# Optimization experiments

Measured on AMD Instinct MI355X. Metric: run time of the kernel, lower is better.

## Reference

```python
import jax, jax.numpy as jnp
import numpy as np

B, S, D = 16, 2048, 128

def setup_inputs() -> dict:
    key = jax.random.key(0)
    kq, kk, kv, km = jax.random.split(key, 4)
    Q = jax.random.normal(kq, (B, S, D), dtype=jnp.float32)
    K = jax.random.normal(kk, (B, S, D), dtype=jnp.float32)
    V = jax.random.normal(kv, (B, S, D), dtype=jnp.float32)
    # mask: True entries are masked out (filled with -inf), same as torch.masked_fill_
    mask = jax.random.randint(km, (B, S, S), 0, 2).astype(bool)
    return {"Q": Q, "K": K, "V": V, "mask": mask, "dk": 128}

def reference(Q, K, V, mask, dk):
    # scores: [B, S_q, S_k]
    w = jnp.einsum('bqd,bkd->bqk', Q, K)
    w = jnp.where(mask, -jnp.inf, w)
    # scale applied to masked scores (as in original: mask first, then divide);
    # -inf / scale stays -inf, so math matches exactly.
    scale = jnp.asarray(dk, w.dtype) ** 0.5
    p = jax.nn.softmax(w / scale, axis=-1)
    # context: [B, S_q, D]
    return jnp.einsum('bqk,bkd->bqd', p, V)
```

## Files before the change

### kernel.cpp

```cpp
#include <hip/hip_runtime.h>
#include <hip/hip_bf16.h>
#include <stdint.h>

typedef __attribute__((ext_vector_type(8))) short short8;
typedef __attribute__((ext_vector_type(4))) float floatx4;

#define S_LEN 2048
#define DH    128
#define BQ    64
#define BKV   64
#define NSTEP (S_LEN / BKV)
#define SCALE 0.08838834764831845f

__device__ __forceinline__ unsigned short f2b(float f) {
    union { float f; unsigned u; } v; v.f = f;
    unsigned r = v.u + 0x7fffu + ((v.u >> 16) & 1u);
    return (unsigned short)(r >> 16);
}

#define LDS_BYTES 77824

__global__ __launch_bounds__(256, 2)
void attn_fwd(const float* __restrict__ Q, const float* __restrict__ K,
              const float* __restrict__ V, const int* __restrict__ M,
              float* __restrict__ O)
{
    __shared__ __align__(128) char lds[LDS_BYTES];

    const int tid  = threadIdx.x;
    const int lane = tid & 63;
    const int w    = tid >> 6;
    const int c    = lane & 15;
    const int g    = lane >> 4;
    const int qt   = blockIdx.x;
    const int b    = blockIdx.y;
    const int q0   = qt * BQ;

    const int rbase = tid >> 5;
    const int c4    = tid & 31;
    const unsigned swk = (unsigned)(c4 * 8) ^ (unsigned)(rbase << 4);
    const int vd    = tid & 127;
    const int vk0   = (tid >> 7) * 32;

    short8 qf[4];
    {
        const float* qrow = Q + ((size_t)(b * S_LEN + q0 + w * 16 + c)) * DH;
        #pragma unroll
        for (int dk = 0; dk < 4; ++dk) {
            const float* p = qrow + dk * 32 + g * 8;
            float4 a  = *(const float4*)(p);
            float4 bb = *(const float4*)(p + 4);
            short8 f;
            f[0] = f2b(a.x * SCALE);  f[1] = f2b(a.y * SCALE);
            f[2] = f2b(a.z * SCALE);  f[3] = f2b(a.w * SCALE);
            f[4] = f2b(bb.x * SCALE); f[5] = f2b(bb.y * SCALE);
            f[6] = f2b(bb.z * SCALE); f[7] = f2b(bb.w * SCALE);
            qf[dk] = f;
        }
    }

    float m_run[4] = {-1e30f, -1e30f, -1e30f, -1e30f};
    float l_run[4] = {0.f, 0.f, 0.f, 0.f};
    floatx4 accO[8];
    #pragma unroll
    for (int i = 0; i < 8; ++i) accO[i] = (floatx4)(0.f);

    const float* Kb = K + (size_t)b * S_LEN * DH;
    const float* Vb = V + (size_t)b * S_LEN * DH;
    const int*   Mb = M + (size_t)b * S_LEN * S_LEN + (size_t)q0 * S_LEN;

    size_t moff[4];
    #pragma unroll
    for (int r = 0; r < 4; ++r)
        moff[r] = (size_t)(w * 16 + 4 * g + r) * S_LEN;

    float4 kreg[8];
    float  vreg[32];
    int    mreg[16];

    #pragma unroll
    for (int i = 0; i < 8; ++i)
        kreg[i] = *(const float4*)(Kb + (size_t)(i * 8 + rbase) * DH + c4 * 4);
    #pragma unroll
    for (int j = 0; j < 32; ++j)
        vreg[j] = Vb[(size_t)(vk0 + j) * DH + vd];
    #pragma unroll
    for (int r = 0; r < 4; ++r)
        #pragma unroll
        for (int n = 0; n < 4; ++n)
            mreg[r * 4 + n] = Mb[moff[r] + n * 16 + c];

    #pragma unroll
    for (int i = 0; i < 8; ++i) {
        float4 kv = kreg[i];
        unsigned long long kp =
              (unsigned long long)f2b(kv.x)
            | ((unsigned long long)f2b(kv.y) << 16)
            | ((unsigned long long)f2b(kv.z) << 32)
            | ((unsigned long long)f2b(kv.w) << 48);
        *(unsigned long long*)(lds + (i * 8 + rbase) * 256 + swk) = kp;
    }
    {
        char* vbase = lds + 32768 + vd * 144 + vk0 * 2;
        #pragma unroll
        for (int i = 0; i < 4; ++i) {
            short8 pk;
            #pragma unroll
            for (int e = 0; e < 8; ++e) pk[e] = f2b(vreg[i * 8 + e]);
            *(short8*)(vbase + i * 16) = pk;
        }
    }
    #pragma unroll
    for (int i = 0; i < 8; ++i)
        kreg[i] = *(const float4*)(Kb + (size_t)(BKV + i * 8 + rbase) * DH + c4 * 4);
    #pragma unroll
    for (int j = 0; j < 32; ++j)
        vreg[j] = Vb[(size_t)(BKV + vk0 + j) * DH + vd];

    __syncthreads();

    char* psw = lds + 69632 + w * 2048;

    for (int step = 0; step < NSTEP; ++step) {
        const int p = step & 1;
        const int kv0 = step * BKV;
        char* KHp = lds + p * 16384;
        char* VTp = lds + 32768 + p * 18432;

        floatx4 accS[4];
        #pragma unroll
        for (int n = 0; n < 4; ++n) accS[n] = (floatx4)(0.f);
        #pragma unroll
        for (int n = 0; n < 4; ++n) {
            const char* krow = KHp + (n * 16 + c) * 256;
            #pragma unroll
            for (int dk = 0; dk < 4; ++dk) {
                unsigned colb = (unsigned)(dk * 64 + g * 16) ^ (unsigned)((c & 7) << 4);
                short8 kf = *(const short8*)(krow + colb);
                accS[n] = __builtin_amdgcn_mfma_f32_16x16x32_bf16(qf[dk], kf, accS[n], 0, 0, 0);
            }
        }

        float pv[4][4];
        float corr[4];
        #pragma unroll
        for (int r = 0; r < 4; ++r) {
            float sv[4];
            #pragma unroll
            for (int n = 0; n < 4; ++n) {
                float s = accS[n][r];
                if (mreg[r * 4 + n]) s = -1e30f;
                sv[n] = s;
            }
            float tm = fmaxf(fmaxf(sv[0], sv[1]), fmaxf(sv[2], sv[3]));
            #pragma unroll
            for (int off = 1; off < 16; off <<= 1)
                tm = fmaxf(tm, __shfl_xor(tm, off, 64));
            float mn = fmaxf(m_run[r], tm);
            corr[r]  = __expf(m_run[r] - mn);
            m_run[r] = mn;
            float ts = 0.f;
            #pragma unroll
            for (int n = 0; n < 4; ++n) { pv[n][r] = __expf(sv[n] - mn); ts += pv[n][r]; }
            #pragma unroll
            for (int off = 1; off < 16; off <<= 1)
                ts += __shfl_xor(ts, off, 64);
            l_run[r] = l_run[r] * corr[r] + ts;
        }
        if (step + 1 < NSTEP) {
            const int kvn = kv0 + BKV;
            #pragma unroll
            for (int r = 0; r < 4; ++r)
                #pragma unroll
                for (int n = 0; n < 4; ++n)
                    mreg[r * 4 + n] = Mb[moff[r] + kvn + n * 16 + c];
        }

        #pragma unroll
        for (int s8 = 0; s8 < 8; ++s8) {
            floatx4 o = accO[s8];
            o[0] *= corr[0]; o[1] *= corr[1]; o[2] *= corr[2]; o[3] *= corr[3];
            accO[s8] = o;
        }

        #pragma unroll
        for (int r = 0; r < 4; ++r) {
            int rl = 4 * g + r;
            #pragma unroll
            for (int n = 0; n < 4; ++n) {
                unsigned colb = (unsigned)((n * 16 + c) * 2) ^ (unsigned)((rl & 7) << 4);
                *(unsigned short*)(psw + rl * 128 + colb) = f2b(pv[n][r]);
            }
        }

        #pragma unroll
        for (int sub = 0; sub < 2; ++sub) {
            unsigned colb = (unsigned)(sub * 64 + g * 16) ^ (unsigned)((c & 7) << 4);
            short8 pf = *(const short8*)(psw + c * 128 + colb);
            #pragma unroll
            for (int s8 = 0; s8 < 8; ++s8) {
                short8 vf = *(const short8*)(VTp + (s8 * 16 + c) * 144 + sub * 64 + g * 16);
                accO[s8] = __builtin_amdgcn_mfma_f32_16x16x32_bf16(pf, vf, accO[s8], 0, 0, 0);
            }
        }

        if (step + 1 < NSTEP) {
            char* KHn = lds + (p ^ 1) * 16384;
            char* VTn = lds + 32768 + (p ^ 1) * 18432;
            #pragma unroll
            for (int i = 0; i < 8; ++i) {
                float4 kv = kreg[i];
                unsigned long long kp =
                      (unsigned long long)f2b(kv.x)
                    | ((unsigned long long)f2b(kv.y) << 16)
                    | ((unsigned long long)f2b(kv.z) << 32)
                    | ((unsigned long long)f2b(kv.w) << 48);
                *(unsigned long long*)(KHn + (i * 8 + rbase) * 256 + swk) = kp;
            }
            char* vbase = VTn + vd * 144 + vk0 * 2;
            #pragma unroll
            for (int i = 0; i < 4; ++i) {
                short8 pk;
                #pragma unroll
                for (int e = 0; e < 8; ++e) pk[e] = f2b(vreg[i * 8 + e]);
                *(short8*)(vbase + i * 16) = pk;
            }
            if (step + 2 < NSTEP) {
                const int kvn2 = kv0 + 2 * BKV;
                #pragma unroll
                for (int i = 0; i < 8; ++i)
                    kreg[i] = *(const float4*)(Kb + (size_t)(kvn2 + i * 8 + rbase) * DH + c4 * 4);
                #pragma unroll
                for (int j = 0; j < 32; ++j)
                    vreg[j] = Vb[(size_t)(kvn2 + vk0 + j) * DH + vd];
            }
        }
        __syncthreads();
    }

    float inv[4];
    #pragma unroll
    for (int r = 0; r < 4; ++r) inv[r] = (l_run[r] > 0.f) ? 1.f / l_run[r] : 0.f;
    float* Ob = O + ((size_t)(b * S_LEN + q0 + w * 16)) * DH;
    #pragma unroll
    for (int s8 = 0; s8 < 8; ++s8) {
        #pragma unroll
        for (int r = 0; r < 4; ++r) {
            Ob[(size_t)(4 * g + r) * DH + s8 * 16 + c] = accO[s8][r] * inv[r];
        }
    }
}

extern "C" void kernel_launch(void* const* d_in, const int* in_sizes, int n_in,
                              void* d_out, int out_size, void* d_ws, size_t ws_size,
                              hipStream_t stream) {
    const float* Q = (const float*)d_in[0];
    const float* K = (const float*)d_in[1];
    const float* V = (const float*)d_in[2];
    const int*   M = (const int*)d_in[3];
    float*       O = (float*)d_out;
    dim3 grid(S_LEN / BQ, 16);
    attn_fwd<<<grid, dim3(256), 0, stream>>>(Q, K, V, M, O);
}
```

Baseline: 131.7 us.

## Pre-convert K to bf16 and pre-transpose V, stream K via global_load_lds

Adds two prep kernels: one converts K to bf16 and one transposes V into a bf16 d-major layout, both written to workspace. The attention kernel then loads K straight into swizzled LDS with global_load_lds double buffering and copies V^T tiles without per-element conversion. This halves K/V bytes re-read by every query tile and removes conversion work from the inner loop, at the cost of two extra launches and a pass over K/V. The old kernel is kept as a fallback when the workspace is too small.

```diff
diff --git a/kernel.cpp b/kernel.cpp
--- a/kernel.cpp
+++ b/kernel.cpp
@@ -18,11 +18,45 @@
     return (unsigned short)(r >> 16);
 }
 
+__device__ __forceinline__ void gll16(const void* g, void* l) {
+    __builtin_amdgcn_global_load_lds(
+        (__attribute__((address_space(1))) void*)(g),
+        (__attribute__((address_space(3))) void*)(l), 16, 0, 0);
+}
+
+
+__global__ __launch_bounds__(256) void conv_k(const float* __restrict__ K,
+                                              unsigned short* __restrict__ Kbf)
+{
+    int i = blockIdx.x * 256 + threadIdx.x;
+    float4 v = ((const float4*)K)[i];
+    ushort4 o;
+    o.x = f2b(v.x); o.y = f2b(v.y); o.z = f2b(v.z); o.w = f2b(v.w);
+    ((ushort4*)Kbf)[i] = o;
+}
+
+__global__ __launch_bounds__(256) void transp_v(const float* __restrict__ V,
+                                                unsigned short* __restrict__ Vt)
+{
+    __shared__ float t[32][33];
+    const int k0 = blockIdx.x * 32, d0 = blockIdx.y * 32, b = blockIdx.z;
+    const int tx = threadIdx.x & 31, ty = threadIdx.x >> 5;
+    const float* Vb = V + ((size_t)b * S_LEN + k0) * DH + d0;
+    #pragma unroll
+    for (int i = 0; i < 4; ++i)
+        t[ty + 8 * i][tx] = Vb[(size_t)(ty + 8 * i) * DH + tx];
+    __syncthreads();
+    unsigned short* Vtb = Vt + ((size_t)b * DH + d0) * S_LEN + k0;
+    #pragma unroll
+    for (int i = 0; i < 4; ++i)
+        Vtb[(size_t)(ty + 8 * i) * S_LEN + tx] = f2b(t[tx][ty + 8 * i]);
+}
+
 #define LDS_BYTES 77824
 
 __global__ __launch_bounds__(256, 2)
-void attn_fwd(const float* __restrict__ Q, const float* __restrict__ K,
-              const float* __restrict__ V, const int* __restrict__ M,
+void attn_fwd(const float* __restrict__ Q, const unsigned short* __restrict__ Kbf,
+              const unsigned short* __restrict__ Vt, const int* __restrict__ M,
               float* __restrict__ O)
 {
     __shared__ __align__(128) char lds[LDS_BYTES];
@@ -36,11 +70,8 @@
     const int b    = blockIdx.y;
     const int q0   = qt * BQ;
 
-    const int rbase = tid >> 5;
-    const int c4    = tid & 31;
-    const unsigned swk = (unsigned)(c4 * 8) ^ (unsigned)(rbase << 4);
-    const int vd    = tid & 127;
-    const int vk0   = (tid >> 7) * 32;
+    const int vd = tid & 127;
+    const int vh = tid >> 7;
 
     short8 qf[4];
     {
@@ -65,6 +96,216 @@
     #pragma unroll
     for (int i = 0; i < 8; ++i) accO[i] = (floatx4)(0.f);
 
+    const unsigned short* Kb  = Kbf + (size_t)b * S_LEN * DH;
+    const unsigned short* Vtb = Vt  + (size_t)b * DH * S_LEN;
+    const int*            Mb  = M   + (size_t)b * S_LEN * S_LEN + (size_t)q0 * S_LEN;
+
+    size_t moff[4];
+    #pragma unroll
+    for (int r = 0; r < 4; ++r)
+        moff[r] = (size_t)(w * 16 + 4 * g + r) * S_LEN;
+
+    short8 vreg[4];
+    int    mreg[16];
+
+    const int krow_l = lane >> 4;
+    const int kcol_l = (lane & 15) * 16;
+
+    #pragma unroll
+    for (int i = 0; i < 4; ++i) {
+        int j = (w << 2) | i;
+        int r = j * 4 + krow_l;
+        unsigned cb = (unsigned)kcol_l ^ (unsigned)((r & 7) << 4);
+        gll16((const char*)Kb + (size_t)r * 256 + cb, lds + j * 1024);
+    }
+    #pragma unroll
+    for (int j = 0; j < 4; ++j)
+        vreg[j] = *(const short8*)(Vtb + (size_t)vd * S_LEN + vh * 32 + j * 8);
+    #pragma unroll
+    for (int j = 0; j < 4; ++j)
+        *(short8*)(lds + 32768 + vd * 144 + vh * 64 + j * 16) = vreg[j];
+    #pragma unroll
+    for (int r = 0; r < 4; ++r)
+        #pragma unroll
+        for (int n = 0; n < 4; ++n)
+            mreg[r * 4 + n] = Mb[moff[r] + n * 16 + c];
+    #pragma unroll
+    for (int j = 0; j < 4; ++j)
+        vreg[j] = *(const short8*)(Vtb + (size_t)vd * S_LEN + BKV + vh * 32 + j * 8);
+
+    __syncthreads();
+
+    char* psw = lds + 69632 + w * 2048;
+
+    for (int step = 0; step < NSTEP; ++step) {
+        const int p = step & 1;
+        const int kv0 = step * BKV;
+        char* KHp = lds + p * 16384;
+        char* VTp = lds + 32768 + p * 18432;
+
+        if (step + 1 < NSTEP) {
+            const char* Ksrc = (const char*)Kb + (size_t)(kv0 + BKV) * 256;
+            char* KHn = lds + (p ^ 1) * 16384;
+            #pragma unroll
+            for (int i = 0; i < 4; ++i) {
+                int j = (w << 2) | i;
+                int r = j * 4 + krow_l;
+                unsigned cb = (unsigned)kcol_l ^ (unsigned)((r & 7) << 4);
+                gll16(Ksrc + (size_t)r * 256 + cb, KHn + j * 1024);
+            }
+        }
+
+        floatx4 accS[4];
+        #pragma unroll
+        for (int n = 0; n < 4; ++n) accS[n] = (floatx4)(0.f);
+        #pragma unroll
+        for (int n = 0; n < 4; ++n) {
+            const char* krow = KHp + (n * 16 + c) * 256;
+            #pragma unroll
+            for (int dk = 0; dk < 4; ++dk) {
+                unsigned colb = (unsigned)(dk * 64 + g * 16) ^ (unsigned)((c & 7) << 4);
+                short8 kf = *(const short8*)(krow + colb);
+                accS[n] = __builtin_amdgcn_mfma_f32_16x16x32_bf16(qf[dk], kf, accS[n], 0, 0, 0);
+            }
+        }
+
+        float pv[4][4];
+        float corr[4];
+        #pragma unroll
+        for (int r = 0; r < 4; ++r) {
+            float sv[4];
+            #pragma unroll
+            for (int n = 0; n < 4; ++n) {
+                float s = accS[n][r];
+                if (mreg[r * 4 + n]) s = -1e30f;
+                sv[n] = s;
+            }
+            float tm = fmaxf(fmaxf(sv[0], sv[1]), fmaxf(sv[2], sv[3]));
+            #pragma unroll
+            for (int off = 1; off < 16; off <<= 1)
+                tm = fmaxf(tm, __shfl_xor(tm, off, 64));
+            float mn = fmaxf(m_run[r], tm);
+            corr[r]  = __expf(m_run[r] - mn);
+            m_run[r] = mn;
+            float ts = 0.f;
+            #pragma unroll
+            for (int n = 0; n < 4; ++n) { pv[n][r] = __expf(sv[n] - mn); ts += pv[n][r]; }
+            #pragma unroll
+            for (int off = 1; off < 16; off <<= 1)
+                ts += __shfl_xor(ts, off, 64);
+            l_run[r] = l_run[r] * corr[r] + ts;
+        }
+        if (step + 1 < NSTEP) {
+            const int kvn = kv0 + BKV;
+            #pragma unroll
+            for (int r = 0; r < 4; ++r)
+                #pragma unroll
+                for (int n = 0; n < 4; ++n)
+                    mreg[r * 4 + n] = Mb[moff[r] + kvn + n * 16 + c];
+        }
+
+        #pragma unroll
+        for (int s8 = 0; s8 < 8; ++s8) {
+            floatx4 o = accO[s8];
+            o[0] *= corr[0]; o[1] *= corr[1]; o[2] *= corr[2]; o[3] *= corr[3];
+            accO[s8] = o;
+        }
+
+        #pragma unroll
+        for (int r = 0; r < 4; ++r) {
+            int rl = 4 * g + r;
+            #pragma unroll
+            for (int n = 0; n < 4; ++n) {
+                unsigned colb = (unsigned)((n * 16 + c) * 2) ^ (unsigned)((rl & 7) << 4);
+                *(unsigned short*)(psw + rl * 128 + colb) = f2b(pv[n][r]);
+            }
+        }
+
+        #pragma unroll
+        for (int sub = 0; sub < 2; ++sub) {
+            unsigned colb = (unsigned)(sub * 64 + g * 16) ^ (unsigned)((c & 7) << 4);
+            short8 pf = *(const short8*)(psw + c * 128 + colb);
+            #pragma unroll
+            for (int s8 = 0; s8 < 8; ++s8) {
+                short8 vf = *(const short8*)(VTp + (s8 * 16 + c) * 144 + sub * 64 + g * 16);
+                accO[s8] = __builtin_amdgcn_mfma_f32_16x16x32_bf16(pf, vf, accO[s8], 0, 0, 0);
+            }
+        }
+
+        if (step + 1 < NSTEP) {
+            char* VTn = lds + 32768 + (p ^ 1) * 18432;
+            #pragma unroll
+            for (int j = 0; j < 4; ++j)
+                *(short8*)(VTn + vd * 144 + vh * 64 + j * 16) = vreg[j];
+            if (step + 2 < NSTEP) {
+                const unsigned short* vsrc = Vtb + (size_t)vd * S_LEN + kv0 + 2 * BKV + vh * 32;
+                #pragma unroll
+                for (int j = 0; j < 4; ++j)
+                    vreg[j] = *(const short8*)(vsrc + j * 8);
+            }
+        }
+        __syncthreads();
+    }
+
+    float inv[4];
+    #pragma unroll
+    for (int r = 0; r < 4; ++r) inv[r] = (l_run[r] > 0.f) ? 1.f / l_run[r] : 0.f;
+    float* Ob = O + ((size_t)(b * S_LEN + q0 + w * 16)) * DH;
+    #pragma unroll
+    for (int s8 = 0; s8 < 8; ++s8) {
+        #pragma unroll
+        for (int r = 0; r < 4; ++r) {
+            Ob[(size_t)(4 * g + r) * DH + s8 * 16 + c] = accO[s8][r] * inv[r];
+        }
+    }
+}
+
+
+__global__ __launch_bounds__(256, 2)
+void attn_fwd_fb(const float* __restrict__ Q, const float* __restrict__ K,
+                 const float* __restrict__ V, const int* __restrict__ M,
+                 float* __restrict__ O)
+{
+    __shared__ __align__(128) char lds[LDS_BYTES];
+
+    const int tid  = threadIdx.x;
+    const int lane = tid & 63;
+    const int w    = tid >> 6;
+    const int c    = lane & 15;
+    const int g    = lane >> 4;
+    const int qt   = blockIdx.x;
+    const int b    = blockIdx.y;
+    const int q0   = qt * BQ;
+
+    const int rbase = tid >> 5;
+    const int c4    = tid & 31;
+    const unsigned swk = (unsigned)(c4 * 8) ^ (unsigned)(rbase << 4);
+    const int vd    = tid & 127;
+    const int vk0   = (tid >> 7) * 32;
+
+    short8 qf[4];
+    {
+        const float* qrow = Q + ((size_t)(b * S_LEN + q0 + w * 16 + c)) * DH;
+        #pragma unroll
+        for (int dk = 0; dk < 4; ++dk) {
+            const float* p = qrow + dk * 32 + g * 8;
+            float4 a  = *(const float4*)(p);
+            float4 bb = *(const float4*)(p + 4);
+            short8 f;
+            f[0] = f2b(a.x * SCALE);  f[1] = f2b(a.y * SCALE);
+            f[2] = f2b(a.z * SCALE);  f[3] = f2b(a.w * SCALE);
+            f[4] = f2b(bb.x * SCALE); f[5] = f2b(bb.y * SCALE);
+            f[6] = f2b(bb.z * SCALE); f[7] = f2b(bb.w * SCALE);
+            qf[dk] = f;
+        }
+    }
+
+    float m_run[4] = {-1e30f, -1e30f, -1e30f, -1e30f};
+    float l_run[4] = {0.f, 0.f, 0.f, 0.f};
+    floatx4 accO[8];
+    #pragma unroll
+    for (int i = 0; i < 8; ++i) accO[i] = (floatx4)(0.f);
+
     const float* Kb = K + (size_t)b * S_LEN * DH;
     const float* Vb = V + (size_t)b * S_LEN * DH;
     const int*   Mb = M + (size_t)b * S_LEN * S_LEN + (size_t)q0 * S_LEN;
@@ -259,6 +500,15 @@
     const float* V = (const float*)d_in[2];
     const int*   M = (const int*)d_in[3];
     float*       O = (float*)d_out;
-    dim3 grid(S_LEN / BQ, 16);
-    attn_fwd<<<grid, dim3(256), 0, stream>>>(Q, K, V, M, O);
-}
+
+    const size_t elems = (size_t)16 * S_LEN * DH;
+    if (ws_size >= 2 * elems * sizeof(unsigned short)) {
+        unsigned short* Kbf = (unsigned short*)d_ws;
+        unsigned short* Vt  = (unsigned short*)d_ws + elems;
+        conv_k<<<dim3((unsigned)(elems / 4 / 256)), dim3(256), 0, stream>>>(K, Kbf);
+        transp_v<<<dim3(S_LEN / 32, DH / 32, 16), dim3(256), 0, stream>>>(V, Vt);
+        attn_fwd<<<dim3(S_LEN / BQ, 16), dim3(256), 0, stream>>>(Q, Kbf, Vt, M, O);
+    } else {
+        attn_fwd_fb<<<dim3(S_LEN / BQ, 16), dim3(256), 0, stream>>>(Q, K, V, M, O);
+    }
+}
```

Measured after the change: 140.3 us. 6.5% more time.

## Pre-convert K to bf16 and transpose V into workspace, async-load K to LDS

Applied to the files above, without the earlier changes.

Adds two pre-pass kernels that convert K to bf16 and write V transposed in bf16 into the workspace. The main attention kernel then streams half-size operands, loads K tiles straight into swizzled LDS with global_load_lds double buffering, and keeps V and the mask in registers one or two steps ahead. It also uses a transposed QK^T MFMA layout so each lane owns one query row, which makes softmax reductions and output stores simpler. LDS use drops and occupancy rises to 3 blocks, at the cost of two extra launches and extra workspace traffic; the old kernel remains as a fallback when the workspace is too small.

```diff
diff --git a/kernel.cpp b/kernel.cpp
--- a/kernel.cpp
+++ b/kernel.cpp
@@ -18,11 +18,51 @@
     return (unsigned short)(r >> 16);
 }
 
-#define LDS_BYTES 77824
-
-__global__ __launch_bounds__(256, 2)
-void attn_fwd(const float* __restrict__ Q, const float* __restrict__ K,
-              const float* __restrict__ V, const int* __restrict__ M,
+__device__ __forceinline__ unsigned cvt_pk(float lo, float hi) {
+    unsigned r;
+    asm("v_cvt_pk_bf16_f32 %0, %1, %2" : "=v"(r) : "v"(lo), "v"(hi));
+    return r;
+}
+
+__device__ __forceinline__ void gll16(const void* g, void* l) {
+    __builtin_amdgcn_global_load_lds(
+        (__attribute__((address_space(1))) void*)(g),
+        (__attribute__((address_space(3))) void*)(l), 16, 0, 0);
+}
+
+
+__global__ __launch_bounds__(256) void conv_k(const float* __restrict__ K,
+                                              unsigned short* __restrict__ Kbf)
+{
+    int i = blockIdx.x * 256 + threadIdx.x;
+    float4 v = ((const float4*)K)[i];
+    ushort4 o;
+    o.x = f2b(v.x); o.y = f2b(v.y); o.z = f2b(v.z); o.w = f2b(v.w);
+    ((ushort4*)Kbf)[i] = o;
+}
+
+__global__ __launch_bounds__(256) void transp_v(const float* __restrict__ V,
+                                                unsigned short* __restrict__ Vt)
+{
+    __shared__ float t[32][33];
+    const int k0 = blockIdx.x * 32, d0 = blockIdx.y * 32, b = blockIdx.z;
+    const int tx = threadIdx.x & 31, ty = threadIdx.x >> 5;
+    const float* Vb = V + ((size_t)b * S_LEN + k0) * DH + d0;
+    #pragma unroll
+    for (int i = 0; i < 4; ++i)
+        t[ty + 8 * i][tx] = Vb[(size_t)(ty + 8 * i) * DH + tx];
+    __syncthreads();
+    unsigned short* Vtb = Vt + ((size_t)b * DH + d0) * S_LEN + k0;
+    #pragma unroll
+    for (int i = 0; i < 4; ++i)
+        Vtb[(size_t)(ty + 8 * i) * S_LEN + tx] = f2b(t[tx][ty + 8 * i]);
+}
+
+#define LDS_BYTES 59392
+
+__global__ __launch_bounds__(256, 3)
+void attn_fwd(const float* __restrict__ Q, const unsigned short* __restrict__ Kbf,
+              const unsigned short* __restrict__ Vt, const int* __restrict__ M,
               float* __restrict__ O)
 {
     __shared__ __align__(128) char lds[LDS_BYTES];
@@ -36,11 +76,10 @@
     const int b    = blockIdx.y;
     const int q0   = qt * BQ;
 
-    const int rbase = tid >> 5;
-    const int c4    = tid & 31;
-    const unsigned swk = (unsigned)(c4 * 8) ^ (unsigned)(rbase << 4);
-    const int vd    = tid & 127;
-    const int vk0   = (tid >> 7) * 32;
+    const int vd = tid & 127;
+    const int vh = tid >> 7;
+    const int krow_l = lane >> 4;
+    const int kcol_l = (lane & 15) * 16;
 
     short8 qf[4];
     {
@@ -59,6 +98,221 @@
         }
     }
 
+    float m_run = -1e30f;
+    float l_run = 0.f;
+    floatx4 accO[8];
+    #pragma unroll
+    for (int i = 0; i < 8; ++i) accO[i] = (floatx4)(0.f);
+
+    const char*           Kb8 = (const char*)(Kbf + (size_t)b * S_LEN * DH);
+    const unsigned short* Vtb = Vt + (size_t)b * DH * S_LEN;
+    const int* Mrow = M + (size_t)b * S_LEN * S_LEN
+                        + (size_t)(q0 + w * 16 + c) * S_LEN + 4 * g;
+
+    short8 vreg[4];
+    int4   mregA[4], mregB[4];
+    char*  psw = lds + 51200 + w * 2048;
+
+#define LOAD_MASK(DST, TT) {                                                  \
+    const int* mp_ = Mrow + (TT) * BKV;                                       \
+    DST[0] = *(const int4*)(mp_);                                             \
+    DST[1] = *(const int4*)(mp_ + 16);                                        \
+    DST[2] = *(const int4*)(mp_ + 32);                                        \
+    DST[3] = *(const int4*)(mp_ + 48); }
+
+    #pragma unroll
+    for (int i = 0; i < 4; ++i) {
+        int j = (w << 2) | i;
+        int r = 4 * j + krow_l;
+        unsigned cb = (unsigned)kcol_l ^ (unsigned)((r & 7) << 4);
+        gll16(Kb8 + (size_t)r * 256 + cb, lds + j * 1024);
+    }
+    #pragma unroll
+    for (int j = 0; j < 4; ++j)
+        vreg[j] = *(const short8*)(Vtb + (size_t)vd * S_LEN + vh * 32 + j * 8);
+    LOAD_MASK(mregA, 0);
+    LOAD_MASK(mregB, 1);
+    __syncthreads();
+
+#define STEP_BODY(T, MCUR) {                                                  \
+    const int pb  = (T) & 1;                                                  \
+    const int kv0 = (T) * BKV;                                                \
+                 \
+    if ((T) + 1 < NSTEP) {                                                    \
+        const char* Ksrc = Kb8 + (size_t)(kv0 + BKV) * 256;                   \
+        char* KHn = lds + ((pb ^ 1) * 16384);                                 \
+        _Pragma("unroll")                                                     \
+        for (int i = 0; i < 4; ++i) {                                         \
+            int j = (w << 2) | i;                                             \
+            int r = 4 * j + krow_l;                                           \
+            unsigned cb = (unsigned)kcol_l ^ (unsigned)((r & 7) << 4);        \
+            gll16(Ksrc + (size_t)r * 256 + cb, KHn + j * 1024);               \
+        }                                                                     \
+    }                                                                         \
+                                           \
+    _Pragma("unroll")                                                         \
+    for (int j = 0; j < 4; ++j)                                               \
+        *(short8*)(lds + 32768 + vd * 144 + vh * 64 + j * 16) = vreg[j];      \
+                                             \
+    if ((T) + 1 < NSTEP) {                                                    \
+        const unsigned short* vs_ = Vtb + (size_t)vd * S_LEN                  \
+                                   + (kv0 + BKV) + vh * 32;                   \
+        _Pragma("unroll")                                                     \
+        for (int j = 0; j < 4; ++j)                                           \
+            vreg[j] = *(const short8*)(vs_ + j * 8);                          \
+    }                                                                         \
+                         \
+    floatx4 accS[4];                                                          \
+    _Pragma("unroll")                                                         \
+    for (int n = 0; n < 4; ++n) accS[n] = (floatx4)(0.f);                     \
+    {                                                                         \
+        const char* KHp = lds + pb * 16384;                                   \
+        _Pragma("unroll")                                                     \
+        for (int n = 0; n < 4; ++n) {                                         \
+            const char* krow = KHp + (n * 16 + c) * 256;                      \
+            _Pragma("unroll")                                                 \
+            for (int dk = 0; dk < 4; ++dk) {                                  \
+                short8 kf = *(const short8*)(krow +                           \
+                    ((unsigned)(dk * 64 + g * 16) ^ (unsigned)((c & 7) << 4)));\
+                accS[n] = __builtin_amdgcn_mfma_f32_16x16x32_bf16(            \
+                              kf, qf[dk], accS[n], 0, 0, 0);                  \
+            }                                                                 \
+        }                                                                     \
+    }                                                                         \
+             \
+    float p_[4][4];                                                           \
+    _Pragma("unroll")                                                         \
+    for (int n = 0; n < 4; ++n) {                                             \
+        int4 mm = MCUR[n];                                                    \
+        p_[n][0] = mm.x ? -1e30f : accS[n][0];                                \
+        p_[n][1] = mm.y ? -1e30f : accS[n][1];                                \
+        p_[n][2] = mm.z ? -1e30f : accS[n][2];                                \
+        p_[n][3] = mm.w ? -1e30f : accS[n][3];                                \
+    }                                                                         \
+    float mx = p_[0][0];                                                      \
+    _Pragma("unroll")                                                         \
+    for (int n = 0; n < 4; ++n)                                               \
+        _Pragma("unroll")                                                     \
+        for (int r = 0; r < 4; ++r) mx = fmaxf(mx, p_[n][r]);                 \
+    mx = fmaxf(mx, __shfl_xor(mx, 16));                                       \
+    mx = fmaxf(mx, __shfl_xor(mx, 32));                                       \
+    float mn   = fmaxf(m_run, mx);                                            \
+    float corr = __expf(m_run - mn);                                          \
+    m_run = mn;                                                               \
+    float ts = 0.f;                                                           \
+    _Pragma("unroll")                                                         \
+    for (int n = 0; n < 4; ++n)                                               \
+        _Pragma("unroll")                                                     \
+        for (int r = 0; r < 4; ++r) {                                         \
+            p_[n][r] = __expf(p_[n][r] - mn);                                 \
+            ts += p_[n][r];                                                   \
+        }                                                                     \
+    ts += __shfl_xor(ts, 16);                                                 \
+    ts += __shfl_xor(ts, 32);                                                 \
+    l_run = l_run * corr + ts;                                                \
+                             \
+    if ((T) + 2 < NSTEP) LOAD_MASK(MCUR, (T) + 2);                            \
+               \
+    _Pragma("unroll")                                                         \
+    for (int n = 0; n < 4; ++n) {                                             \
+        unsigned w0 = cvt_pk(p_[n][0], p_[n][1]);                             \
+        unsigned w1 = cvt_pk(p_[n][2], p_[n][3]);                             \
+        unsigned long long pk = (unsigned long long)w0                        \
+                              | ((unsigned long long)w1 << 32);               \
+        *(unsigned long long*)(psw + (4 * n + g) * 128                        \
+                               + ((c * 8) ^ (g << 3))) = pk;                  \
+    }                                                                         \
+                                     \
+    _Pragma("unroll")                                                         \
+    for (int s8 = 0; s8 < 8; ++s8) {                                          \
+        floatx4 o = accO[s8];                                                 \
+        o[0] *= corr; o[1] *= corr; o[2] *= corr; o[3] *= corr;               \
+        accO[s8] = o;                                                         \
+    }                                                                         \
+                                    \
+    asm volatile("s_waitcnt lgkmcnt(0)" ::: "memory");                        \
+    __builtin_amdgcn_s_barrier();                                             \
+                                              \
+    _Pragma("unroll")                                                         \
+    for (int sub = 0; sub < 2; ++sub) {                                       \
+        int ra = 8 * sub + 2 * g;                                             \
+        unsigned long long lo = *(const unsigned long long*)(psw + ra * 128   \
+                                + ((c * 8) ^ ((ra & 3) << 3)));               \
+        unsigned long long hi = *(const unsigned long long*)(psw + (ra+1)*128 \
+                                + ((c * 8) ^ (((ra + 1) & 3) << 3)));         \
+        union { unsigned long long q[2]; short8 v; } pu;                      \
+        pu.q[0] = lo; pu.q[1] = hi;                                           \
+        short8 pf = pu.v;                                                     \
+        _Pragma("unroll")                                                     \
+        for (int s8 = 0; s8 < 8; ++s8) {                                      \
+            short8 vf = *(const short8*)(lds + 32768 + (s8 * 16 + c) * 144    \
+                                         + sub * 64 + g * 16);                \
+            accO[s8] = __builtin_amdgcn_mfma_f32_16x16x32_bf16(               \
+                           vf, pf, accO[s8], 0, 0, 0);                        \
+        }                                                                     \
+    }                                                                         \
+                                                               \
+    __syncthreads(); }
+
+    for (int t = 0; t < NSTEP; t += 2) {
+        STEP_BODY(t,     mregA)
+        STEP_BODY(t + 1, mregB)
+    }
+#undef STEP_BODY
+#undef LOAD_MASK
+
+    float inv = (l_run > 0.f) ? 1.f / l_run : 0.f;
+    float* Ob = O + ((size_t)(b * S_LEN + q0 + w * 16 + c)) * DH;
+    #pragma unroll
+    for (int s8 = 0; s8 < 8; ++s8) {
+        float4 ov;
+        ov.x = accO[s8][0] * inv; ov.y = accO[s8][1] * inv;
+        ov.z = accO[s8][2] * inv; ov.w = accO[s8][3] * inv;
+        *(float4*)(Ob + s8 * 16 + 4 * g) = ov;
+    }
+}
+
+#define FB_LDS_BYTES 77824
+
+__global__ __launch_bounds__(256, 2)
+void attn_fwd_fb(const float* __restrict__ Q, const float* __restrict__ K,
+                 const float* __restrict__ V, const int* __restrict__ M,
+                 float* __restrict__ O)
+{
+    __shared__ __align__(128) char lds[FB_LDS_BYTES];
+
+    const int tid  = threadIdx.x;
+    const int lane = tid & 63;
+    const int w    = tid >> 6;
+    const int c    = lane & 15;
+    const int g    = lane >> 4;
+    const int qt   = blockIdx.x;
+    const int b    = blockIdx.y;
+    const int q0   = qt * BQ;
+
+    const int rbase = tid >> 5;
+    const int c4    = tid & 31;
+    const unsigned swk = (unsigned)(c4 * 8) ^ (unsigned)(rbase << 4);
+    const int vd    = tid & 127;
+    const int vk0   = (tid >> 7) * 32;
+
+    short8 qf[4];
+    {
+        const float* qrow = Q + ((size_t)(b * S_LEN + q0 + w * 16 + c)) * DH;
+        #pragma unroll
+        for (int dk = 0; dk < 4; ++dk) {
+            const float* p = qrow + dk * 32 + g * 8;
+            float4 a  = *(const float4*)(p);
+            float4 bb = *(const float4*)(p + 4);
+            short8 f;
+            f[0] = f2b(a.x * SCALE);  f[1] = f2b(a.y * SCALE);
+            f[2] = f2b(a.z * SCALE);  f[3] = f2b(a.w * SCALE);
+            f[4] = f2b(bb.x * SCALE); f[5] = f2b(bb.y * SCALE);
+            f[6] = f2b(bb.z * SCALE); f[7] = f2b(bb.w * SCALE);
+            qf[dk] = f;
+        }
+    }
+
     float m_run[4] = {-1e30f, -1e30f, -1e30f, -1e30f};
     float l_run[4] = {0.f, 0.f, 0.f, 0.f};
     floatx4 accO[8];
@@ -259,6 +513,15 @@
     const float* V = (const float*)d_in[2];
     const int*   M = (const int*)d_in[3];
     float*       O = (float*)d_out;
-    dim3 grid(S_LEN / BQ, 16);
-    attn_fwd<<<grid, dim3(256), 0, stream>>>(Q, K, V, M, O);
-}
+
+    const size_t elems = (size_t)16 * S_LEN * DH;
+    if (ws_size >= 2 * elems * sizeof(unsigned short)) {
+        unsigned short* Kbf = (unsigned short*)d_ws;
+        unsigned short* Vt  = (unsigned short*)d_ws + elems;
+        conv_k<<<dim3((unsigned)(elems / 4 / 256)), dim3(256), 0, stream>>>(K, Kbf);
+        transp_v<<<dim3(S_LEN / 32, DH / 32, 16), dim3(256), 0, stream>>>(V, Vt);
+        attn_fwd<<<dim3(S_LEN / BQ, 16), dim3(256), 0, stream>>>(Q, Kbf, Vt, M, O);
+    } else {
+        attn_fwd_fb<<<dim3(S_LEN / BQ, 16), dim3(256), 0, stream>>>(Q, K, V, M, O);
+    }
+}
```

Measured after the change: 121.6 us. 1.08x faster.
